# Kernel optimization log

Hardware: AMD Instinct MI355X
Metric: run time of the kernel (lower is better)

Reference implementation:

```python
import jax, jax.numpy as jnp
import numpy as np

SIGMA = 0.01        # config['fscore_sigma']
FSCORE_W = 0.1      # config['fscore_weight']
TASK_W = 1.0        # config['task_weight']
DOMAIN_W = 0.1      # config['domain_weight']


def setup_inputs() -> dict:
    key = jax.random.key(0)
    ks = jax.random.split(key, 11)
    B, N, M, F = 8, 4096, 4096, 512
    H1, H2, D = 256, 128, 6
    return {
        "pred_pc": jax.random.normal(ks[0], (B, N, 3), jnp.float32),
        "target_pc": jax.random.normal(ks[1], (B, M, 3), jnp.float32),
        "domain_features": jax.random.normal(ks[2], (B, F), jnp.float32),
        "dataset_weights": jax.random.uniform(ks[3], (B,), jnp.float32, 0.9, 1.2),
        "W1": jax.random.normal(ks[4], (F, H1), jnp.float32) * 0.02,
        "b1": jnp.zeros((H1,), jnp.float32),
        "W2": jax.random.normal(ks[5], (H1, H2), jnp.float32) * 0.02,
        "b2": jnp.zeros((H2,), jnp.float32),
        "W3": jax.random.normal(ks[6], (H2, D), jnp.float32) * 0.02,
        "b3": jnp.zeros((D,), jnp.float32),
        "domain_labels": jax.random.randint(ks[7], (B,), 0, D),
    }


def _chamfer_mins(pred, tgt):
    # pred: [B,N,3], tgt: [B,M,3] -> squared pairwise dists [B,N,M], then dual mins
    d = (jnp.sum(pred ** 2, axis=2)[:, :, None]
         + jnp.sum(tgt ** 2, axis=2)[:, None, :]
         - 2.0 * jnp.einsum('bnd,bmd->bnm', pred, tgt))
    return jnp.min(d, axis=2), jnp.min(d, axis=1)   # [B,N], [B,M]


def reference(pred_pc, target_pc, domain_features, dataset_weights,
              W1, b1, W2, b2, W3, b3, domain_labels):
    min_a, min_b = _chamfer_mins(pred_pc, target_pc)
    c = 2.0 * SIGMA * SIGMA
    soft_a = jnp.exp(-min_a / c)
    soft_b = jnp.exp(-min_b / c)

    # batch-level task loss (compute_reconstruction_loss on full batch)
    chamfer = jnp.mean(min_a) + jnp.mean(min_b)
    prec = jnp.mean(soft_a)
    rec = jnp.mean(soft_b)
    fscore = 2.0 * prec * rec / (prec + rec + 1e-8)
    task = chamfer + FSCORE_W * (1.0 - fscore)

    # per-sample dataset-weighted loss (vectorized form of the Python loop)
    ch_i = jnp.mean(min_a, axis=1) + jnp.mean(min_b, axis=1)
    p_i = jnp.mean(soft_a, axis=1)
    r_i = jnp.mean(soft_b, axis=1)
    f_i = 2.0 * p_i * r_i / (p_i + r_i + 1e-8)
    loss_i = ch_i + FSCORE_W * (1.0 - f_i)
    dataset_weighted = jnp.mean(dataset_weights * loss_i)

    # domain loss: GRL is identity in forward; classifier in eval mode (dropout off)
    h = jax.nn.relu(domain_features @ W1 + b1)
    h = jax.nn.relu(h @ W2 + b2)
    logits = h @ W3 + b3
    logp = jax.nn.log_softmax(logits, axis=-1)
    domain = -jnp.mean(jnp.take_along_axis(logp, domain_labels[:, None], axis=1))

    total = TASK_W * task + DOMAIN_W * domain + dataset_weighted
    return total
```

## Files before the change

### kernel.cpp

```cpp
#include <hip/hip_runtime.h>
#include <math.h>

#define B 8
#define NPTS 4096
#define SPLITS 32
#define LOG2S 5
#define REFS (NPTS / SPLITS)
#define QPT 8
#define THREADS 256


__device__ __forceinline__ void final_combine_atomic(
    float* sums32, float* nlls, const float* w, float* out) {
  float chamfer = 0.f, prec = 0.f, rec = 0.f, dsw = 0.f, dom = 0.f;
  for (int b = 0; b < B; ++b) {
    float sa  = atomicAdd(&sums32[(0 * B + b) * 2 + 0], 0.f);
    float ssa = atomicAdd(&sums32[(0 * B + b) * 2 + 1], 0.f);
    float sb  = atomicAdd(&sums32[(1 * B + b) * 2 + 0], 0.f);
    float ssb = atomicAdd(&sums32[(1 * B + b) * 2 + 1], 0.f);
    float nb  = atomicAdd(&nlls[b], 0.f);
    float ma = sa / 4096.f, mb = sb / 4096.f;
    float p = ssa / 4096.f, r = ssb / 4096.f;
    chamfer += ma + mb;
    prec += p; rec += r;
    float f_i = 2.f * p * r / (p + r + 1e-8f);
    float loss_i = ma + mb + 0.1f * (1.f - f_i);
    dsw += w[b] * loss_i;
    dom += nb;
  }
  chamfer *= (1.f / B); prec *= (1.f / B); rec *= (1.f / B);
  dsw *= (1.f / B); dom *= (1.f / B);
  float fscore = 2.f * prec * rec / (prec + rec + 1e-8f);
  float task = chamfer + 0.1f * (1.f - fscore);
  out[0] = 1.0f * task + 0.1f * dom + dsw;
}

__global__ __launch_bounds__(THREADS, 4) void k_main(
    const float* __restrict__ pred, const float* __restrict__ targ,
    const float* __restrict__ x, const float* __restrict__ W1,
    float* __restrict__ partial, float* __restrict__ sums32,
    float* __restrict__ h1p, unsigned int* __restrict__ cnt) {
  int id = blockIdx.x, tid = threadIdx.x;
  __shared__ float4 sbuf4[REFS];

  if (id >= 1024) {
    if (id == 1088) {
      if (tid < 32) sums32[tid] = 0.f;
      if (tid == 0) cnt[0] = 0u;
      return;
    }
    int lid = id - 1024;
    int b = lid >> 3, kc = lid & 7;
    float* xs = (float*)sbuf4;
    if (tid < 64) xs[tid] = x[b * 512 + kc * 64 + tid];
    __syncthreads();
    float acc = 0.f;
    const float* w = W1 + (size_t)(kc * 64) * 256 + tid;
#pragma unroll 8
    for (int k = 0; k < 64; ++k) acc = fmaf(xs[k], w[k * 256], acc);
    h1p[(b * 8 + kc) * 256 + tid] = acc;
    return;
  }

  int split  = id & (SPLITS - 1);
  int qchunk = (id >> LOG2S) & 1;
  int b      = (id >> (LOG2S + 1)) & 7;
  int dir    = id >> (LOG2S + 4);
  const float* qp = dir ? targ : pred;
  const float* rp = dir ? pred : targ;

  float4* refs = sbuf4;
  const float* rb = rp + ((size_t)b * NPTS + (size_t)split * REFS) * 3;
  for (int i = tid; i < REFS; i += THREADS) {
    float xx = rb[i * 3 + 0], yy = rb[i * 3 + 1], zz = rb[i * 3 + 2];
    refs[i] = make_float4(xx, yy, zz, 0.5f * (xx * xx + yy * yy + zz * zz));
  }
  __syncthreads();

  const float* qb = qp + (size_t)b * NPTS * 3;
  int q0 = qchunk * (QPT * THREADS) + tid;
  float qx[QPT], qy[QPT], qz[QPT], vmin[QPT];
#pragma unroll
  for (int i = 0; i < QPT; ++i) {
    int q = q0 + i * THREADS;
    qx[i] = qb[q * 3 + 0];
    qy[i] = qb[q * 3 + 1];
    qz[i] = qb[q * 3 + 2];
    vmin[i] = 3.4e38f;
  }

  float4 t0 = refs[0], t1 = refs[1], t2 = refs[2], t3 = refs[3];
  asm volatile("" : "+v"(t0.x), "+v"(t0.y), "+v"(t0.z), "+v"(t0.w),
                    "+v"(t1.x), "+v"(t1.y), "+v"(t1.z), "+v"(t1.w),
                    "+v"(t2.x), "+v"(t2.y), "+v"(t2.z), "+v"(t2.w),
                    "+v"(t3.x), "+v"(t3.y), "+v"(t3.z), "+v"(t3.w));
  for (int j = 0; j < REFS; j += 4) {
    int jn = (j + 4) & (REFS - 1);
    float4 n0 = refs[jn + 0], n1 = refs[jn + 1];
    float4 n2 = refs[jn + 2], n3 = refs[jn + 3];
#pragma unroll
    for (int i = 0; i < QPT; ++i) {
      float s0 = fmaf(-qx[i], t0.x, fmaf(-qy[i], t0.y, fmaf(-qz[i], t0.z, t0.w)));
      float s1 = fmaf(-qx[i], t1.x, fmaf(-qy[i], t1.y, fmaf(-qz[i], t1.z, t1.w)));
      float s2 = fmaf(-qx[i], t2.x, fmaf(-qy[i], t2.y, fmaf(-qz[i], t2.z, t2.w)));
      float s3 = fmaf(-qx[i], t3.x, fmaf(-qy[i], t3.y, fmaf(-qz[i], t3.z, t3.w)));
      vmin[i] = fminf(fminf(vmin[i], fminf(s0, s1)), fminf(s2, s3));
    }
    asm volatile("" : "+v"(n0.x), "+v"(n0.y), "+v"(n0.z), "+v"(n0.w),
                      "+v"(n1.x), "+v"(n1.y), "+v"(n1.z), "+v"(n1.w),
                      "+v"(n2.x), "+v"(n2.y), "+v"(n2.z), "+v"(n2.w),
                      "+v"(n3.x), "+v"(n3.y), "+v"(n3.z), "+v"(n3.w));
    t0 = n0; t1 = n1; t2 = n2; t3 = n3;
  }

  size_t base = (((size_t)dir * B + b) * SPLITS + split) * NPTS;
#pragma unroll
  for (int i = 0; i < QPT; ++i) {
    float qn = fmaf(qx[i], qx[i], fmaf(qy[i], qy[i], qz[i] * qz[i]));
    partial[base + q0 + i * THREADS] = fmaf(2.f, vmin[i], qn);
  }
}

__global__ __launch_bounds__(THREADS) void k_finish(
    const float* __restrict__ partial, float* __restrict__ sums32,
    const float* __restrict__ h1p, const float* __restrict__ b1,
    const float* __restrict__ W2, const float* __restrict__ b2,
    const float* __restrict__ W3, const float* __restrict__ b3,
    const int* __restrict__ labels, const float* __restrict__ wgt,
    float* __restrict__ nlls, unsigned int* __restrict__ cnt,
    float* __restrict__ out) {
  int id = blockIdx.x, tid = threadIdx.x;
  __shared__ float sbuf[4160];
  __shared__ unsigned int sflag;

  if (id < 64) {
    int dirb  = id >> 2;
    int chunk = id & 3;
    const float* pbase = partial + (size_t)dirb * SPLITS * NPTS
                       + (size_t)chunk * 1024 + (size_t)tid * 4;
    float4 m4 = make_float4(3.4e38f, 3.4e38f, 3.4e38f, 3.4e38f);
#pragma unroll
    for (int s = 0; s < SPLITS; ++s) {
      float4 v = *(const float4*)(pbase + (size_t)s * NPTS);
      m4.x = fminf(m4.x, v.x); m4.y = fminf(m4.y, v.y);
      m4.z = fminf(m4.z, v.z); m4.w = fminf(m4.w, v.w);
    }
    float s_min  = (m4.x + m4.y) + (m4.z + m4.w);
    float s_soft = (__expf(-5000.0f * m4.x) + __expf(-5000.0f * m4.y))
                 + (__expf(-5000.0f * m4.z) + __expf(-5000.0f * m4.w));
    for (int off = 32; off > 0; off >>= 1) {
      s_min  += __shfl_down(s_min,  off);
      s_soft += __shfl_down(s_soft, off);
    }
    int wave = tid >> 6, lane = tid & 63;
    if (lane == 0) { sbuf[wave * 2] = s_min; sbuf[wave * 2 + 1] = s_soft; }
    __syncthreads();
    if (tid == 0) {
      float a = 0.f, c = 0.f;
      for (int w = 0; w < 4; ++w) { a += sbuf[w * 2]; c += sbuf[w * 2 + 1]; }
      float o0 = atomicAdd(&sums32[dirb * 2 + 0], a);
      float o1 = atomicAdd(&sums32[dirb * 2 + 1], c);
      asm volatile("" :: "v"(o0), "v"(o1));
      unsigned int old = atomicAdd(cnt, 1u);
      sflag = (old == 64u) ? 1u : 0u;
    }
    __syncthreads();
    if (sflag && tid == 0) final_combine_atomic(sums32, nlls, wgt, out);
    return;
  }

  float* h1s = sbuf;
  float* pp  = sbuf + 2048;
  float* lg  = sbuf + 4096;
  for (int i = tid; i < 2048; i += THREADS) {
    int bb = i >> 8, j = i & 255;
    float a = b1[j];
#pragma unroll
    for (int kc = 0; kc < 8; ++kc) a += h1p[(bb * 8 + kc) * 256 + j];
    h1s[i] = fmaxf(a, 0.f);
  }
  __syncthreads();
  {
    int j = tid & 127, half = tid >> 7;
    float acc[8];
#pragma unroll
    for (int bb = 0; bb < 8; ++bb) acc[bb] = 0.f;
    const float* w = W2 + (size_t)(half * 128) * 128 + j;
    for (int k = 0; k < 128; ++k) {
      float wv = w[k * 128];
      int kk = half * 128 + k;
#pragma unroll
      for (int bb = 0; bb < 8; ++bb)
        acc[bb] = fmaf(h1s[bb * 256 + kk], wv, acc[bb]);
    }
#pragma unroll
    for (int bb = 0; bb < 8; ++bb) pp[(half * 8 + bb) * 128 + j] = acc[bb];
  }
  __syncthreads();
  float* h2s = sbuf;
  for (int i = tid; i < 1024; i += THREADS) {
    int bb = i >> 7, j = i & 127;
    float a = b2[j] + pp[(0 * 8 + bb) * 128 + j] + pp[(1 * 8 + bb) * 128 + j];
    h2s[i] = fmaxf(a, 0.f);
  }
  __syncthreads();
  if (tid < 48) {
    int bb = tid / 6, d = tid % 6;
    float acc = b3[d];
#pragma unroll 8
    for (int k = 0; k < 128; ++k) acc = fmaf(h2s[bb * 128 + k], W3[k * 6 + d], acc);
    lg[tid] = acc;
  }
  __syncthreads();
  if (tid < 8) {
    int bb = tid;
    float mx = lg[bb * 6];
    for (int d = 1; d < 6; ++d) mx = fmaxf(mx, lg[bb * 6 + d]);
    float se = 0.f;
    for (int d = 0; d < 6; ++d) se += __expf(lg[bb * 6 + d] - mx);
    int lab = labels[bb];
    float old = atomicExch(&nlls[bb], -(lg[bb * 6 + lab] - mx - __logf(se)));
    asm volatile("" :: "v"(old));
  }
  __syncthreads();
  if (tid == 0) {
    unsigned int old = atomicAdd(cnt, 1u);
    sflag = (old == 64u) ? 1u : 0u;
  }
  __syncthreads();
  if (sflag && tid == 0) final_combine_atomic(sums32, nlls, wgt, out);
}

extern "C" void kernel_launch(void* const* d_in, const int* in_sizes, int n_in,
                              void* d_out, int out_size, void* d_ws, size_t ws_size,
                              hipStream_t stream) {
  const float* pred   = (const float*)d_in[0];
  const float* targ   = (const float*)d_in[1];
  const float* x      = (const float*)d_in[2];
  const float* wgt    = (const float*)d_in[3];
  const float* W1     = (const float*)d_in[4];
  const float* b1     = (const float*)d_in[5];
  const float* W2     = (const float*)d_in[6];
  const float* b2     = (const float*)d_in[7];
  const float* W3     = (const float*)d_in[8];
  const float* b3     = (const float*)d_in[9];
  const int*   labels = (const int*)d_in[10];
  float* out = (float*)d_out;
  char* ws = (char*)d_ws;

  float* partial = (float*)ws;
  float* sums32  = partial + (size_t)2 * B * SPLITS * NPTS;
  float* h1p     = sums32 + 32;
  float* nlls    = h1p + 64 * 256;
  unsigned int* cnt = (unsigned int*)(nlls + 8);

  hipLaunchKernelGGL(k_main, dim3(1089), dim3(THREADS), 0, stream,
                     pred, targ, x, W1, partial, sums32, h1p, cnt);
  hipLaunchKernelGGL(k_finish, dim3(65), dim3(THREADS), 0, stream,
                     partial, sums32, h1p, b1, W2, b2, W3, b3, labels, wgt,
                     nlls, cnt, out);
}
```

Before: 123.5 us.

## Template split count, give each block all queries, move final combine to its own kernel

Each main block now processes all 4096 queries of a batch (16 per thread) against a reference slice, with the number of splits (64/32/16) chosen by workspace size. The register prefetch of the next reference float4 group is removed in favour of loading inside the loop. The last-block atomic counter and the final combine are replaced by a separate single-thread third kernel, which drops the atomics but adds a launch. With 64 splits the partial buffer doubles, so the reduction in k_finish reads twice as much data.

```diff
diff --git a/kernel.cpp b/kernel.cpp
--- a/kernel.cpp
+++ b/kernel.cpp
@@ -3,53 +3,26 @@
 
 #define B 8
 #define NPTS 4096
-#define SPLITS 32
-#define LOG2S 5
-#define REFS (NPTS / SPLITS)
-#define QPT 8
+#define QPT 16
 #define THREADS 256
 
 
-__device__ __forceinline__ void final_combine_atomic(
-    float* sums32, float* nlls, const float* w, float* out) {
-  float chamfer = 0.f, prec = 0.f, rec = 0.f, dsw = 0.f, dom = 0.f;
-  for (int b = 0; b < B; ++b) {
-    float sa  = atomicAdd(&sums32[(0 * B + b) * 2 + 0], 0.f);
-    float ssa = atomicAdd(&sums32[(0 * B + b) * 2 + 1], 0.f);
-    float sb  = atomicAdd(&sums32[(1 * B + b) * 2 + 0], 0.f);
-    float ssb = atomicAdd(&sums32[(1 * B + b) * 2 + 1], 0.f);
-    float nb  = atomicAdd(&nlls[b], 0.f);
-    float ma = sa / 4096.f, mb = sb / 4096.f;
-    float p = ssa / 4096.f, r = ssb / 4096.f;
-    chamfer += ma + mb;
-    prec += p; rec += r;
-    float f_i = 2.f * p * r / (p + r + 1e-8f);
-    float loss_i = ma + mb + 0.1f * (1.f - f_i);
-    dsw += w[b] * loss_i;
-    dom += nb;
-  }
-  chamfer *= (1.f / B); prec *= (1.f / B); rec *= (1.f / B);
-  dsw *= (1.f / B); dom *= (1.f / B);
-  float fscore = 2.f * prec * rec / (prec + rec + 1e-8f);
-  float task = chamfer + 0.1f * (1.f - fscore);
-  out[0] = 1.0f * task + 0.1f * dom + dsw;
-}
-
+template<int S, int LOG2S>
 __global__ __launch_bounds__(THREADS, 4) void k_main(
     const float* __restrict__ pred, const float* __restrict__ targ,
     const float* __restrict__ x, const float* __restrict__ W1,
     float* __restrict__ partial, float* __restrict__ sums32,
-    float* __restrict__ h1p, unsigned int* __restrict__ cnt) {
+    float* __restrict__ h1p) {
+  constexpr int REFS = NPTS / S;
   int id = blockIdx.x, tid = threadIdx.x;
-  __shared__ float4 sbuf4[REFS];
-
-  if (id >= 1024) {
-    if (id == 1088) {
+  __shared__ float4 sbuf4[REFS < 64 ? 64 : REFS];
+
+  if (id >= 16 * S) {
+    if (id == 16 * S + 64) {
       if (tid < 32) sums32[tid] = 0.f;
-      if (tid == 0) cnt[0] = 0u;
       return;
     }
-    int lid = id - 1024;
+    int lid = id - 16 * S;
     int b = lid >> 3, kc = lid & 7;
     float* xs = (float*)sbuf4;
     if (tid < 64) xs[tid] = x[b * 512 + kc * 64 + tid];
@@ -62,10 +35,9 @@
     return;
   }
 
-  int split  = id & (SPLITS - 1);
-  int qchunk = (id >> LOG2S) & 1;
-  int b      = (id >> (LOG2S + 1)) & 7;
-  int dir    = id >> (LOG2S + 4);
+  int split = id & (S - 1);
+  int b     = (id >> LOG2S) & 7;
+  int dir   = id >> (LOG2S + 3);
   const float* qp = dir ? targ : pred;
   const float* rp = dir ? pred : targ;
 
@@ -78,26 +50,23 @@
   __syncthreads();
 
   const float* qb = qp + (size_t)b * NPTS * 3;
-  int q0 = qchunk * (QPT * THREADS) + tid;
   float qx[QPT], qy[QPT], qz[QPT], vmin[QPT];
 #pragma unroll
   for (int i = 0; i < QPT; ++i) {
-    int q = q0 + i * THREADS;
+    int q = tid + i * THREADS;
     qx[i] = qb[q * 3 + 0];
     qy[i] = qb[q * 3 + 1];
     qz[i] = qb[q * 3 + 2];
     vmin[i] = 3.4e38f;
   }
 
-  float4 t0 = refs[0], t1 = refs[1], t2 = refs[2], t3 = refs[3];
-  asm volatile("" : "+v"(t0.x), "+v"(t0.y), "+v"(t0.z), "+v"(t0.w),
-                    "+v"(t1.x), "+v"(t1.y), "+v"(t1.z), "+v"(t1.w),
-                    "+v"(t2.x), "+v"(t2.y), "+v"(t2.z), "+v"(t2.w),
-                    "+v"(t3.x), "+v"(t3.y), "+v"(t3.z), "+v"(t3.w));
   for (int j = 0; j < REFS; j += 4) {
-    int jn = (j + 4) & (REFS - 1);
-    float4 n0 = refs[jn + 0], n1 = refs[jn + 1];
-    float4 n2 = refs[jn + 2], n3 = refs[jn + 3];
+    float4 t0 = refs[j + 0], t1 = refs[j + 1];
+    float4 t2 = refs[j + 2], t3 = refs[j + 3];
+    asm volatile("" : "+v"(t0.x), "+v"(t0.y), "+v"(t0.z), "+v"(t0.w),
+                      "+v"(t1.x), "+v"(t1.y), "+v"(t1.z), "+v"(t1.w),
+                      "+v"(t2.x), "+v"(t2.y), "+v"(t2.z), "+v"(t2.w),
+                      "+v"(t3.x), "+v"(t3.y), "+v"(t3.z), "+v"(t3.w));
 #pragma unroll
     for (int i = 0; i < QPT; ++i) {
       float s0 = fmaf(-qx[i], t0.x, fmaf(-qy[i], t0.y, fmaf(-qz[i], t0.z, t0.w)));
@@ -106,41 +75,34 @@
       float s3 = fmaf(-qx[i], t3.x, fmaf(-qy[i], t3.y, fmaf(-qz[i], t3.z, t3.w)));
       vmin[i] = fminf(fminf(vmin[i], fminf(s0, s1)), fminf(s2, s3));
     }
-    asm volatile("" : "+v"(n0.x), "+v"(n0.y), "+v"(n0.z), "+v"(n0.w),
-                      "+v"(n1.x), "+v"(n1.y), "+v"(n1.z), "+v"(n1.w),
-                      "+v"(n2.x), "+v"(n2.y), "+v"(n2.z), "+v"(n2.w),
-                      "+v"(n3.x), "+v"(n3.y), "+v"(n3.z), "+v"(n3.w));
-    t0 = n0; t1 = n1; t2 = n2; t3 = n3;
-  }
-
-  size_t base = (((size_t)dir * B + b) * SPLITS + split) * NPTS;
+  }
+
+  size_t base = (((size_t)dir * B + b) * S + split) * NPTS;
 #pragma unroll
   for (int i = 0; i < QPT; ++i) {
     float qn = fmaf(qx[i], qx[i], fmaf(qy[i], qy[i], qz[i] * qz[i]));
-    partial[base + q0 + i * THREADS] = fmaf(2.f, vmin[i], qn);
-  }
-}
-
+    partial[base + tid + i * THREADS] = fmaf(2.f, vmin[i], qn);
+  }
+}
+
+template<int S>
 __global__ __launch_bounds__(THREADS) void k_finish(
     const float* __restrict__ partial, float* __restrict__ sums32,
     const float* __restrict__ h1p, const float* __restrict__ b1,
     const float* __restrict__ W2, const float* __restrict__ b2,
     const float* __restrict__ W3, const float* __restrict__ b3,
-    const int* __restrict__ labels, const float* __restrict__ wgt,
-    float* __restrict__ nlls, unsigned int* __restrict__ cnt,
-    float* __restrict__ out) {
+    const int* __restrict__ labels, float* __restrict__ nlls) {
   int id = blockIdx.x, tid = threadIdx.x;
   __shared__ float sbuf[4160];
-  __shared__ unsigned int sflag;
 
   if (id < 64) {
     int dirb  = id >> 2;
     int chunk = id & 3;
-    const float* pbase = partial + (size_t)dirb * SPLITS * NPTS
+    const float* pbase = partial + (size_t)dirb * S * NPTS
                        + (size_t)chunk * 1024 + (size_t)tid * 4;
     float4 m4 = make_float4(3.4e38f, 3.4e38f, 3.4e38f, 3.4e38f);
-#pragma unroll
-    for (int s = 0; s < SPLITS; ++s) {
+#pragma unroll 8
+    for (int s = 0; s < S; ++s) {
       float4 v = *(const float4*)(pbase + (size_t)s * NPTS);
       m4.x = fminf(m4.x, v.x); m4.y = fminf(m4.y, v.y);
       m4.z = fminf(m4.z, v.z); m4.w = fminf(m4.w, v.w);
@@ -158,14 +120,9 @@
     if (tid == 0) {
       float a = 0.f, c = 0.f;
       for (int w = 0; w < 4; ++w) { a += sbuf[w * 2]; c += sbuf[w * 2 + 1]; }
-      float o0 = atomicAdd(&sums32[dirb * 2 + 0], a);
-      float o1 = atomicAdd(&sums32[dirb * 2 + 1], c);
-      asm volatile("" :: "v"(o0), "v"(o1));
-      unsigned int old = atomicAdd(cnt, 1u);
-      sflag = (old == 64u) ? 1u : 0u;
-    }
-    __syncthreads();
-    if (sflag && tid == 0) final_combine_atomic(sums32, nlls, wgt, out);
+      atomicAdd(&sums32[dirb * 2 + 0], a);
+      atomicAdd(&sums32[dirb * 2 + 1], c);
+    }
     return;
   }
 
@@ -219,16 +176,53 @@
     float se = 0.f;
     for (int d = 0; d < 6; ++d) se += __expf(lg[bb * 6 + d] - mx);
     int lab = labels[bb];
-    float old = atomicExch(&nlls[bb], -(lg[bb * 6 + lab] - mx - __logf(se)));
-    asm volatile("" :: "v"(old));
-  }
-  __syncthreads();
-  if (tid == 0) {
-    unsigned int old = atomicAdd(cnt, 1u);
-    sflag = (old == 64u) ? 1u : 0u;
-  }
-  __syncthreads();
-  if (sflag && tid == 0) final_combine_atomic(sums32, nlls, wgt, out);
+    nlls[bb] = -(lg[bb * 6 + lab] - mx - __logf(se));
+  }
+}
+
+__global__ __launch_bounds__(64) void k_combine(
+    const float* __restrict__ sums32, const float* __restrict__ nlls,
+    const float* __restrict__ w, float* __restrict__ out) {
+  if (threadIdx.x != 0) return;
+  float chamfer = 0.f, prec = 0.f, rec = 0.f, dsw = 0.f, dom = 0.f;
+  for (int b = 0; b < B; ++b) {
+    float sa  = sums32[(0 * B + b) * 2 + 0];
+    float ssa = sums32[(0 * B + b) * 2 + 1];
+    float sb  = sums32[(1 * B + b) * 2 + 0];
+    float ssb = sums32[(1 * B + b) * 2 + 1];
+    float ma = sa / 4096.f, mb = sb / 4096.f;
+    float p = ssa / 4096.f, r = ssb / 4096.f;
+    chamfer += ma + mb;
+    prec += p; rec += r;
+    float f_i = 2.f * p * r / (p + r + 1e-8f);
+    float loss_i = ma + mb + 0.1f * (1.f - f_i);
+    dsw += w[b] * loss_i;
+    dom += nlls[b];
+  }
+  chamfer *= (1.f / B); prec *= (1.f / B); rec *= (1.f / B);
+  dsw *= (1.f / B); dom *= (1.f / B);
+  float fscore = 2.f * prec * rec / (prec + rec + 1e-8f);
+  float task = chamfer + 0.1f * (1.f - fscore);
+  out[0] = 1.0f * task + 0.1f * dom + dsw;
+}
+
+template<int S, int LOG2S>
+static void run_pipeline(const float* pred, const float* targ, const float* x,
+                         const float* wgt, const float* W1, const float* b1,
+                         const float* W2, const float* b2, const float* W3,
+                         const float* b3, const int* labels, float* out,
+                         char* ws, hipStream_t stream) {
+  float* partial = (float*)ws;
+  float* sums32  = partial + (size_t)2 * B * S * NPTS;
+  float* h1p     = sums32 + 32;
+  float* nlls    = h1p + 64 * 256;
+
+  hipLaunchKernelGGL((k_main<S, LOG2S>), dim3(16 * S + 65), dim3(THREADS), 0,
+                     stream, pred, targ, x, W1, partial, sums32, h1p);
+  hipLaunchKernelGGL((k_finish<S>), dim3(65), dim3(THREADS), 0, stream,
+                     partial, sums32, h1p, b1, W2, b2, W3, b3, labels, nlls);
+  hipLaunchKernelGGL(k_combine, dim3(1), dim3(64), 0, stream,
+                     sums32, nlls, wgt, out);
 }
 
 extern "C" void kernel_launch(void* const* d_in, const int* in_sizes, int n_in,
@@ -248,15 +242,16 @@
   float* out = (float*)d_out;
   char* ws = (char*)d_ws;
 
-  float* partial = (float*)ws;
-  float* sums32  = partial + (size_t)2 * B * SPLITS * NPTS;
-  float* h1p     = sums32 + 32;
-  float* nlls    = h1p + 64 * 256;
-  unsigned int* cnt = (unsigned int*)(nlls + 8);
-
-  hipLaunchKernelGGL(k_main, dim3(1089), dim3(THREADS), 0, stream,
-                     pred, targ, x, W1, partial, sums32, h1p, cnt);
-  hipLaunchKernelGGL(k_finish, dim3(65), dim3(THREADS), 0, stream,
-                     partial, sums32, h1p, b1, W2, b2, W3, b3, labels, wgt,
-                     nlls, cnt, out);
-}
+  auto need = [](int S) {
+    return ((size_t)2 * B * S * NPTS + 32 + 64 * 256 + 8) * sizeof(float);
+  };
+  if (ws_size >= need(64))
+    run_pipeline<64, 6>(pred, targ, x, wgt, W1, b1, W2, b2, W3, b3, labels,
+                        out, ws, stream);
+  else if (ws_size >= need(32))
+    run_pipeline<32, 5>(pred, targ, x, wgt, W1, b1, W2, b2, W3, b3, labels,
+                        out, ws, stream);
+  else
+    run_pipeline<16, 4>(pred, targ, x, wgt, W1, b1, W2, b2, W3, b3, labels,
+                        out, ws, stream);
+}
```

Result: faster. 114.1 us (-7.7%).
